# Performance work log

Hardware: AMD Instinct MI355X
Metric: run time of the kernel (lower is better)

The kernel has to match this reference:

```python
import jax, jax.numpy as jnp
import numpy as np

B, LQ, LA, D, H = 8, 2048, 2048, 300, 150

def setup_inputs() -> dict:
    key = jax.random.key(0)
    ks = jax.random.split(key, 6)
    return {
        "Q": jax.random.normal(ks[0], (B, LQ, D), dtype=jnp.float32),
        "A": jax.random.normal(ks[1], (B, LA, D), dtype=jnp.float32),
        "Wi": jax.random.normal(ks[2], (D, H), dtype=jnp.float32) * (1.0 / np.sqrt(D)),
        "Wu": jax.random.normal(ks[3], (D, H), dtype=jnp.float32) * (1.0 / np.sqrt(D)),
        "Wg": jax.random.normal(ks[4], (H, H), dtype=jnp.float32) * (1.0 / np.sqrt(H)),
        "Wt": jax.random.normal(ks[5], (2 * H, H), dtype=jnp.float32) * (1.0 / np.sqrt(2 * H)),
        "bi": jnp.zeros((H,), dtype=jnp.float32),
        "bu": jnp.zeros((H,), dtype=jnp.float32),
        "bg": jnp.zeros((H,), dtype=jnp.float32),
        "bt": jnp.zeros((H,), dtype=jnp.float32),
    }

def reference(Q, A, Wi, Wu, Wg, Wt, bi, bu, bg, bt):
    # sigmoid/tanh gated projections (shared weights for Q and A)
    def gate(X):
        return jax.nn.sigmoid(X @ Wi + bi) * jnp.tanh(X @ Wu + bu)
    Qh = gate(Q)  # [B, LQ, H]
    Ah = gate(A)  # [B, LA, H]
    # attention scores G[b,q,a] = <(Qh Wg + bg)[b,q], Ah[b,a]>
    G = jnp.einsum('bqh,bah->bqa', Qh @ Wg + bg, Ah)
    G = jax.nn.softmax(G, axis=1)  # softmax over Q positions
    # H[b,a] = sum_q G[b,q,a] * Qh[b,q]
    Hm = jnp.einsum('bqa,bqh->bah', G, Qh)  # [B, LA, H]
    # 'nn' comparison: relu(concat([Ah, Hm]) @ Wt + bt)
    T = jax.nn.relu(jnp.concatenate([Ah, Hm], axis=-1) @ Wt + bt)
    return T
```

## Files before the change

kernel.cpp:

```cpp
#include <hip/hip_runtime.h>
#include <math.h>

#define BB 8
#define LQ 2048
#define DD 300
#define HHH 150
#define NROWS (BB * LQ)

#define KP 168
#define QTS 72
#define XSS 328
#define WCE 27136
#define JT 144
#define SLAB_B 45056
#define SLAB_E 22528
#define QHT_OFF_E 11008

typedef __bf16 bf16x8 __attribute__((ext_vector_type(8)));
typedef __bf16 bf16x4 __attribute__((ext_vector_type(4)));
typedef float f32x16 __attribute__((ext_vector_type(16)));

__device__ __forceinline__ void gl_lds16(const void* g, void* l) {
    __builtin_amdgcn_global_load_lds(
        (const __attribute__((address_space(1))) void*)g,
        (__attribute__((address_space(3))) void*)l,
        16, 0, 0);
}
__device__ __forceinline__ void stage_flat(const void* g, void* l, int bytes,
                                           int w, int lane) {
    for (int ofs = w * 1024; ofs < bytes; ofs += 4096)
        gl_lds16((const char*)g + ofs + lane * 16, (char*)l + ofs);
}
__device__ __forceinline__ f32x16 z16() {
    f32x16 v;
#pragma unroll
    for (int i = 0; i < 16; i++) v[i] = 0.f;
    return v;
}

__global__ __launch_bounds__(256) void convert_weights(
    const float* __restrict__ Wi, const float* __restrict__ Wu,
    const float* __restrict__ Wg, const float* __restrict__ Wt,
    __bf16* __restrict__ WiC, __bf16* __restrict__ WuC,
    __bf16* __restrict__ WgT, __bf16* __restrict__ Wt12)
{
    const int z = blockIdx.y;
    const int i = blockIdx.x * 256 + threadIdx.x;
    if (z < 2) {
        if (i >= 2 * WCE) return;
        int c = i / WCE, rem = i - c * WCE;
        float v = 0.f;
        if (rem < 160 * KP) {
            int h = rem / KP, kc = rem - h * KP;
            int d = c * 160 + kc;
            if (kc < 160 && d < DD && h < HHH) v = (z ? Wu : Wi)[(size_t)d * HHH + h];
        }
        (z ? WuC : WiC)[i] = (__bf16)v;
    } else if (z == 2) {
        if (i >= WCE) return;
        float v = 0.f;
        if (i < 160 * KP) {
            int h = i / KP, kc = i - h * KP;
            if (kc < HHH && h < HHH) v = Wg[(size_t)kc * HHH + h];
        }
        WgT[i] = (__bf16)v;
    } else {
        if (i >= 2 * 160 * KP) return;
        int c = i / (160 * KP), rem = i - c * (160 * KP);
        int h = rem / KP, kc = rem - h * KP;
        float v = (kc < HHH && h < HHH) ? Wt[(size_t)(c * HHH + kc) * HHH + h] : 0.f;
        Wt12[i] = (__bf16)v;
    }
}

__global__ __launch_bounds__(256, 1) void gatep(
    const float* __restrict__ Q, const float* __restrict__ A,
    const __bf16* __restrict__ WiC, const __bf16* __restrict__ WuC,
    const __bf16* __restrict__ WgT,
    const float* __restrict__ bi, const float* __restrict__ bu,
    const float* __restrict__ bg,
    __bf16* __restrict__ AhB, __bf16* __restrict__ Slab)
{
    __shared__ __align__(16) __bf16 Xs[128 * XSS];
    __shared__ __align__(16) __bf16 WS[WCE];
    const int tid = threadIdx.x;
    const int w = tid >> 6, lane = tid & 63;
    const int m32 = lane & 31, half = lane >> 5;
    const int z = blockIdx.y;
    const int r0 = blockIdx.x * 128;
    const float* X = z ? A : Q;

    stage_flat(WiC, WS, 54272, w, lane);

    const float4* xs4 = (const float4*)(X + (size_t)r0 * DD);
    for (int i = tid; i < 9600; i += 256) {
        int row = i / 75, c4 = (i - row * 75) * 4;
        float4 v = xs4[i];
        *(bf16x4*)(Xs + row * XSS + c4) =
            (bf16x4){(__bf16)v.x, (__bf16)v.y, (__bf16)v.z, (__bf16)v.w};
    }
    for (int i = tid; i < 128 * 7; i += 256) {
        int row = i / 7, c4 = 300 + (i - row * 7) * 4;
        *(bf16x4*)(Xs + row * XSS + c4) =
            (bf16x4){(__bf16)0.f, (__bf16)0.f, (__bf16)0.f, (__bf16)0.f};
    }
    __syncthreads();

    f32x16 ai[5], au[5];
#pragma unroll
    for (int t = 0; t < 5; t++) { ai[t] = z16(); au[t] = z16(); }
    bf16x8 af[10];

    for (int c = 0; c < 2; c++) {
        if (c) { __syncthreads(); stage_flat(WiC + WCE, WS, 54272, w, lane); __syncthreads(); }
#pragma unroll
        for (int ks = 0; ks < 10; ks++)
            af[ks] = *(const bf16x8*)(Xs + (w * 32 + m32) * XSS + c * 160 + ks * 16 + half * 8);
        for (int ks = 0; ks < 10; ks++)
#pragma unroll
            for (int t = 0; t < 5; t++)
                ai[t] = __builtin_amdgcn_mfma_f32_32x32x16_bf16(
                    af[ks], *(const bf16x8*)(WS + (t * 32 + m32) * KP + ks * 16 + half * 8),
                    ai[t], 0, 0, 0);
        __syncthreads();
        stage_flat(WuC + (size_t)c * WCE, WS, 54272, w, lane);
        __syncthreads();
        for (int ks = 0; ks < 10; ks++)
#pragma unroll
            for (int t = 0; t < 5; t++)
                au[t] = __builtin_amdgcn_mfma_f32_32x32x16_bf16(
                    af[ks], *(const bf16x8*)(WS + (t * 32 + m32) * KP + ks * 16 + half * 8),
                    au[t], 0, 0, 0);
    }

#pragma unroll
    for (int t = 0; t < 5; t++) {
        int h = t * 32 + m32;
        int hc = h < HHH ? h : 0;
        float bih = bi[hc], buh = bu[hc];
#pragma unroll
        for (int r = 0; r < 16; r++) {
            float v = 0.f;
            if (h < HHH) {
                float xi = ai[t][r] + bih, xu = au[t][r] + buh;
                v = (1.f / (1.f + __expf(-xi))) * tanhf(xu);
            }
            ai[t][r] = v;
        }
    }

    if (z) {
#pragma unroll
        for (int t = 0; t < 5; t++) {
            int h = t * 32 + m32;
#pragma unroll
            for (int r = 0; r < 16; r++) {
                int rowp = (r & 3) + 8 * (r >> 2) + 4 * half;
                AhB[(size_t)(r0 + w * 32 + rowp) * KP + h] = (__bf16)ai[t][r];
            }
        }
        return;
    }

    __syncthreads();
#pragma unroll
    for (int t = 0; t < 5; t++) {
        int h = t * 32 + m32;
#pragma unroll
        for (int r = 0; r < 16; r++) {
            int rowp = (r & 3) + 8 * (r >> 2) + 4 * half;
            int j = w * 32 + rowp;
            __bf16 v = (__bf16)ai[t][r];
            Xs[j * KP + h] = v;
            WS[h * JT + j] = v;
        }
    }
    __syncthreads();
    const int b = r0 >> 11, qt0 = (r0 & 2047) >> 6;
    for (int i = tid; i < 2560; i += 256) {
        int tile = i / 1280, rr = i - tile * 1280;
        int hh = rr >> 3, seg = rr & 7;
        *(bf16x8*)(Slab + (size_t)(b * 32 + qt0 + tile) * SLAB_E + QHT_OFF_E + hh * QTS + seg * 8)
            = *(const bf16x8*)(WS + hh * JT + tile * 64 + seg * 8);
    }
    __syncthreads();
    stage_flat(WgT, WS, 54272, w, lane);
    __syncthreads();

    bf16x8 af2[10];
#pragma unroll
    for (int ks = 0; ks < 10; ks++)
        af2[ks] = *(const bf16x8*)(Xs + (w * 32 + m32) * KP + ks * 16 + half * 8);
    f32x16 qg[5];
#pragma unroll
    for (int t = 0; t < 5; t++) qg[t] = z16();
    for (int ks = 0; ks < 10; ks++)
#pragma unroll
        for (int t = 0; t < 5; t++)
            qg[t] = __builtin_amdgcn_mfma_f32_32x32x16_bf16(
                af2[ks], *(const bf16x8*)(WS + (t * 32 + m32) * KP + ks * 16 + half * 8),
                qg[t], 0, 0, 0);

#pragma unroll
    for (int t = 0; t < 5; t++) {
        int h = t * 32 + m32;
        int hc = h < HHH ? h : 0;
        float bgh = bg[hc];
#pragma unroll
        for (int r = 0; r < 16; r++) {
            int rowp = (r & 3) + 8 * (r >> 2) + 4 * half;
            int q = (r0 & 2047) + w * 32 + rowp;
            float v = (h < HHH) ? (qg[t][r] + bgh) : 0.f;
            Slab[(size_t)(b * 32 + (q >> 6)) * SLAB_E + (q & 63) * KP + h] = (__bf16)v;
        }
    }
}

__global__ __launch_bounds__(256, 1) void attn_mfma(
    const __bf16* __restrict__ Slab, const __bf16* __restrict__ AhB,
    __bf16* __restrict__ O, float* __restrict__ L)
{
    __shared__ __align__(16) __bf16 AhS[128 * KP];
    __shared__ __align__(16) __bf16 Buf[2][SLAB_E];
    __shared__ __align__(16) __bf16 PS[128 * QTS];
    const int tid = threadIdx.x;
    const int w = tid >> 6, lane = tid & 63;
    const int m32 = lane & 31, half = lane >> 5;
    const int b = blockIdx.y, qh = blockIdx.z;
    const int a0 = blockIdx.x * 128;

    stage_flat(AhB + (size_t)(b * LQ + a0) * KP, AhS, 43008, w, lane);
    const char* slabBase = (const char*)Slab + (size_t)(b * 32 + qh * 16) * SLAB_B;
    stage_flat(slabBase, Buf[0], SLAB_B, w, lane);
    __syncthreads();

    bf16x8 af[10];
#pragma unroll
    for (int ks = 0; ks < 10; ks++)
        af[ks] = *(const bf16x8*)(AhS + (w * 32 + m32) * KP + ks * 16 + half * 8);

    float lsum[16];
#pragma unroll
    for (int r = 0; r < 16; r++) lsum[r] = 0.f;
    f32x16 acc[5];
#pragma unroll
    for (int t = 0; t < 5; t++) acc[t] = z16();

    for (int qt = 0; qt < 16; qt++) {
        const int cur = qt & 1;
        if (qt < 15)
            stage_flat(slabBase + (size_t)(qt + 1) * SLAB_B, Buf[cur ^ 1], SLAB_B, w, lane);
        const __bf16* Bq = Buf[cur];
        const __bf16* Bv = Buf[cur] + QHT_OFF_E;

        f32x16 s0 = z16(), s1 = z16();
        for (int ks = 0; ks < 10; ks++) {
            s0 = __builtin_amdgcn_mfma_f32_32x32x16_bf16(
                af[ks], *(const bf16x8*)(Bq + m32 * KP + ks * 16 + half * 8), s0, 0, 0, 0);
            s1 = __builtin_amdgcn_mfma_f32_32x32x16_bf16(
                af[ks], *(const bf16x8*)(Bq + (32 + m32) * KP + ks * 16 + half * 8), s1, 0, 0, 0);
        }
#pragma unroll
        for (int r = 0; r < 16; r++) {
            int rowp = (r & 3) + 8 * (r >> 2) + 4 * half;
            float p0 = __expf(s0[r]);
            float p1 = __expf(s1[r]);
            lsum[r] += p0 + p1;
            PS[(w * 32 + rowp) * QTS + m32] = (__bf16)p0;
            PS[(w * 32 + rowp) * QTS + 32 + m32] = (__bf16)p1;
        }
#pragma unroll
        for (int kk = 0; kk < 4; kk++) {
            bf16x8 pf = *(const bf16x8*)(PS + (w * 32 + m32) * QTS + kk * 16 + half * 8);
#pragma unroll
            for (int t = 0; t < 5; t++)
                acc[t] = __builtin_amdgcn_mfma_f32_32x32x16_bf16(
                    pf, *(const bf16x8*)(Bv + (t * 32 + m32) * QTS + kk * 16 + half * 8),
                    acc[t], 0, 0, 0);
        }
        __syncthreads();
    }

#pragma unroll
    for (int r = 0; r < 16; r++) {
        float s = lsum[r];
#pragma unroll
        for (int m = 1; m < 32; m <<= 1) s += __shfl_xor(s, m, 64);
        lsum[r] = s;
    }
    __bf16* Ob = O + (size_t)(qh * NROWS + b * LQ + a0) * 160;
#pragma unroll
    for (int t = 0; t < 5; t++) {
        int h = t * 32 + m32;
#pragma unroll
        for (int r = 0; r < 16; r++) {
            int rowp = (r & 3) + 8 * (r >> 2) + 4 * half;
            Ob[(size_t)(w * 32 + rowp) * 160 + h] = (__bf16)acc[t][r];
        }
    }
    if (m32 == 0) {
        float* Lb = L + qh * NROWS + b * LQ + a0 + w * 32;
#pragma unroll
        for (int r = 0; r < 16; r++) {
            int rowp = (r & 3) + 8 * (r >> 2) + 4 * half;
            Lb[rowp] = lsum[r];
        }
    }
}

__global__ __launch_bounds__(256, 1) void final_mfma(
    const __bf16* __restrict__ AhB, const __bf16* __restrict__ O,
    const float* __restrict__ L, const __bf16* __restrict__ Wt12,
    const float* __restrict__ bt, float* __restrict__ Out)
{
    __shared__ __align__(16) __bf16 AS[64 * KP];
    __shared__ __align__(16) __bf16 HS[64 * KP];
    __shared__ __align__(16) __bf16 WtS[2 * 160 * KP];
    const int tid = threadIdx.x;
    const int w = tid >> 6, lane = tid & 63;
    const int m32 = lane & 31, half = lane >> 5;
    const int r0 = blockIdx.x * 64;

    stage_flat(AhB + (size_t)r0 * KP, AS, 21504, w, lane);
    stage_flat(Wt12, WtS, 107520, w, lane);

    {
        int rhat = tid >> 2, qq = tid & 3;
        int grow = r0 + rhat;
        float inv = 1.f / (L[grow] + L[NROWS + grow]);
        const bf16x8* o1 = (const bf16x8*)(O + (size_t)grow * 160 + qq * 40);
        const bf16x8* o2 = (const bf16x8*)(O + (size_t)(NROWS + grow) * 160 + qq * 40);
#pragma unroll
        for (int k = 0; k < 5; k++) {
            bf16x8 x = o1[k], y = o2[k], hv;
#pragma unroll
            for (int j = 0; j < 8; j++)
                hv[j] = (__bf16)(((float)x[j] + (float)y[j]) * inv);
            *(bf16x8*)(HS + rhat * KP + qq * 40 + k * 8) = hv;
        }
    }
    __syncthreads();

    const int m = w & 1, th = w >> 1;
    const int tbase = th ? 3 : 0, tn = th ? 2 : 3;
    f32x16 acc[3];
#pragma unroll
    for (int i = 0; i < 3; i++) acc[i] = z16();

    for (int ch = 0; ch < 2; ch++) {
        const __bf16* src = ch ? HS : AS;
        for (int ks = 0; ks < 10; ks++) {
            bf16x8 af = *(const bf16x8*)(src + (m * 32 + m32) * KP + ks * 16 + half * 8);
#pragma unroll
            for (int ti = 0; ti < 3; ti++) {
                if (ti < tn) {
                    int t = tbase + ti;
                    acc[ti] = __builtin_amdgcn_mfma_f32_32x32x16_bf16(
                        af, *(const bf16x8*)(WtS + (ch * 160 + t * 32 + m32) * KP + ks * 16 + half * 8),
                        acc[ti], 0, 0, 0);
                }
            }
        }
    }

#pragma unroll
    for (int ti = 0; ti < 3; ti++) {
        if (ti < tn) {
            int t = tbase + ti;
            int h = t * 32 + m32;
            if (h < HHH) {
                float bth = bt[h];
#pragma unroll
                for (int r = 0; r < 16; r++) {
                    int rowp = (r & 3) + 8 * (r >> 2) + 4 * half;
                    float v = acc[ti][r] + bth;
                    Out[(size_t)(r0 + m * 32 + rowp) * HHH + h] = v > 0.f ? v : 0.f;
                }
            }
        }
    }
}

extern "C" void kernel_launch(void* const* d_in, const int* in_sizes, int n_in,
                              void* d_out, int out_size, void* d_ws, size_t ws_size,
                              hipStream_t stream)
{
    const float* Q  = (const float*)d_in[0];
    const float* A  = (const float*)d_in[1];
    const float* Wi = (const float*)d_in[2];
    const float* Wu = (const float*)d_in[3];
    const float* Wg = (const float*)d_in[4];
    const float* Wt = (const float*)d_in[5];
    const float* bi = (const float*)d_in[6];
    const float* bu = (const float*)d_in[7];
    const float* bg = (const float*)d_in[8];
    const float* bt = (const float*)d_in[9];
    float* out = (float*)d_out;

    char* ws = (char*)d_ws;
    __bf16* Slab = (__bf16*)(ws);
    __bf16* AhB  = (__bf16*)(ws + 11534336);
    __bf16* Op   = (__bf16*)(ws + 17039360);
    float*  Lp   = (float*) (ws + 27525120);
    __bf16* WiC  = (__bf16*)(ws + 27656192);
    __bf16* WuC  = (__bf16*)(ws + 27764736);
    __bf16* WgT  = (__bf16*)(ws + 27873280);
    __bf16* Wt12 = (__bf16*)(ws + 27927552);

    convert_weights<<<dim3(212, 4), 256, 0, stream>>>(Wi, Wu, Wg, Wt,
                                                      WiC, WuC, WgT, Wt12);
    gatep<<<dim3(NROWS / 128, 2), 256, 0, stream>>>(Q, A, WiC, WuC, WgT,
                                                    bi, bu, bg, AhB, Slab);
    attn_mfma<<<dim3(16, BB, 2), 256, 0, stream>>>(Slab, AhB, Op, Lp);
    final_mfma<<<NROWS / 64, 256, 0, stream>>>(AhB, Op, Lp, Wt12, bt, out);
}
```

Baseline: 188.5 us.

## Double-buffer gate weights in LDS and load X fragments directly into registers

The gatep kernel now streams X rows straight from global memory into bf16 MFMA fragments instead of staging them through a padded LDS tile. Wi, Wu and Wg chunks are double-buffered in two LDS slabs, so the next weight chunk loads while the current one is used in MFMAs, and several barriers are dropped. tanh is replaced by an exp-based formula, and the transposed Qh slab is written from a single LDS copy with scattered stores. The risks are higher register pressure from holding 20 fragments, uncoalesced direct global loads, and strided 2-byte scatter stores for the transpose.

```diff
diff --git a/kernel.cpp b/kernel.cpp
--- a/kernel.cpp
+++ b/kernel.cpp
@@ -9,9 +9,7 @@
 
 #define KP 168
 #define QTS 72
-#define XSS 328
 #define WCE 27136
-#define JT 144
 #define SLAB_B 45056
 #define SLAB_E 22528
 #define QHT_OFF_E 11008
@@ -36,6 +34,10 @@
 #pragma unroll
     for (int i = 0; i < 16; i++) v[i] = 0.f;
     return v;
+}
+__device__ __forceinline__ bf16x8 cvt8(float4 u, float4 v) {
+    return (bf16x8){(__bf16)u.x, (__bf16)u.y, (__bf16)u.z, (__bf16)u.w,
+                    (__bf16)v.x, (__bf16)v.y, (__bf16)v.z, (__bf16)v.w};
 }
 
 __global__ __launch_bounds__(256) void convert_weights(
@@ -81,8 +83,8 @@
     const float* __restrict__ bg,
     __bf16* __restrict__ AhB, __bf16* __restrict__ Slab)
 {
-    __shared__ __align__(16) __bf16 Xs[128 * XSS];
-    __shared__ __align__(16) __bf16 WS[WCE];
+    __shared__ __align__(16) __bf16 WB[2][WCE];
+    __shared__ __align__(16) __bf16 QhA[128 * KP];
     const int tid = threadIdx.x;
     const int w = tid >> 6, lane = tid & 63;
     const int m32 = lane & 31, half = lane >> 5;
@@ -90,48 +92,68 @@
     const int r0 = blockIdx.x * 128;
     const float* X = z ? A : Q;
 
-    stage_flat(WiC, WS, 54272, w, lane);
-
-    const float4* xs4 = (const float4*)(X + (size_t)r0 * DD);
-    for (int i = tid; i < 9600; i += 256) {
-        int row = i / 75, c4 = (i - row * 75) * 4;
-        float4 v = xs4[i];
-        *(bf16x4*)(Xs + row * XSS + c4) =
-            (bf16x4){(__bf16)v.x, (__bf16)v.y, (__bf16)v.z, (__bf16)v.w};
-    }
-    for (int i = tid; i < 128 * 7; i += 256) {
-        int row = i / 7, c4 = 300 + (i - row * 7) * 4;
-        *(bf16x4*)(Xs + row * XSS + c4) =
-            (bf16x4){(__bf16)0.f, (__bf16)0.f, (__bf16)0.f, (__bf16)0.f};
-    }
-    __syncthreads();
+    stage_flat(WiC, WB[0], 54272, w, lane);
+
+    const float* xrow = X + (size_t)(r0 + w * 32 + m32) * DD + half * 8;
+    bf16x8 af0[10], af1[10];
+#pragma unroll
+    for (int ks = 0; ks < 10; ks++) {
+        float4 u = *(const float4*)(xrow + ks * 16);
+        float4 v = *(const float4*)(xrow + ks * 16 + 4);
+        af0[ks] = cvt8(u, v);
+    }
 
     f32x16 ai[5], au[5];
 #pragma unroll
     for (int t = 0; t < 5; t++) { ai[t] = z16(); au[t] = z16(); }
-    bf16x8 af[10];
-
-    for (int c = 0; c < 2; c++) {
-        if (c) { __syncthreads(); stage_flat(WiC + WCE, WS, 54272, w, lane); __syncthreads(); }
-#pragma unroll
-        for (int ks = 0; ks < 10; ks++)
-            af[ks] = *(const bf16x8*)(Xs + (w * 32 + m32) * XSS + c * 160 + ks * 16 + half * 8);
-        for (int ks = 0; ks < 10; ks++)
-#pragma unroll
-            for (int t = 0; t < 5; t++)
-                ai[t] = __builtin_amdgcn_mfma_f32_32x32x16_bf16(
-                    af[ks], *(const bf16x8*)(WS + (t * 32 + m32) * KP + ks * 16 + half * 8),
-                    ai[t], 0, 0, 0);
-        __syncthreads();
-        stage_flat(WuC + (size_t)c * WCE, WS, 54272, w, lane);
-        __syncthreads();
-        for (int ks = 0; ks < 10; ks++)
-#pragma unroll
-            for (int t = 0; t < 5; t++)
-                au[t] = __builtin_amdgcn_mfma_f32_32x32x16_bf16(
-                    af[ks], *(const bf16x8*)(WS + (t * 32 + m32) * KP + ks * 16 + half * 8),
-                    au[t], 0, 0, 0);
-    }
+
+    __syncthreads();
+    stage_flat(WuC, WB[1], 54272, w, lane);
+
+#pragma unroll
+    for (int ks = 0; ks < 8; ks++) {
+        float4 u = *(const float4*)(xrow + 160 + ks * 16);
+        float4 v = *(const float4*)(xrow + 160 + ks * 16 + 4);
+        af1[ks] = cvt8(u, v);
+    }
+    {
+        float4 u = *(const float4*)(xrow + 288);
+        float4 v = (half == 0) ? *(const float4*)(xrow + 292) : (float4){0.f, 0.f, 0.f, 0.f};
+        af1[8] = cvt8(u, v);
+        af1[9] = (bf16x8){(__bf16)0.f, (__bf16)0.f, (__bf16)0.f, (__bf16)0.f,
+                          (__bf16)0.f, (__bf16)0.f, (__bf16)0.f, (__bf16)0.f};
+    }
+
+    for (int ks = 0; ks < 10; ks++)
+#pragma unroll
+        for (int t = 0; t < 5; t++)
+            ai[t] = __builtin_amdgcn_mfma_f32_32x32x16_bf16(
+                af0[ks], *(const bf16x8*)(WB[0] + (t * 32 + m32) * KP + ks * 16 + half * 8),
+                ai[t], 0, 0, 0);
+    __syncthreads();
+    stage_flat(WiC + WCE, WB[0], 54272, w, lane);
+    for (int ks = 0; ks < 10; ks++)
+#pragma unroll
+        for (int t = 0; t < 5; t++)
+            au[t] = __builtin_amdgcn_mfma_f32_32x32x16_bf16(
+                af0[ks], *(const bf16x8*)(WB[1] + (t * 32 + m32) * KP + ks * 16 + half * 8),
+                au[t], 0, 0, 0);
+    __syncthreads();
+    stage_flat(WuC + WCE, WB[1], 54272, w, lane);
+    for (int ks = 0; ks < 10; ks++)
+#pragma unroll
+        for (int t = 0; t < 5; t++)
+            ai[t] = __builtin_amdgcn_mfma_f32_32x32x16_bf16(
+                af1[ks], *(const bf16x8*)(WB[0] + (t * 32 + m32) * KP + ks * 16 + half * 8),
+                ai[t], 0, 0, 0);
+    __syncthreads();
+    if (z == 0) stage_flat(WgT, WB[0], 54272, w, lane);
+    for (int ks = 0; ks < 10; ks++)
+#pragma unroll
+        for (int t = 0; t < 5; t++)
+            au[t] = __builtin_amdgcn_mfma_f32_32x32x16_bf16(
+                af1[ks], *(const bf16x8*)(WB[1] + (t * 32 + m32) * KP + ks * 16 + half * 8),
+                au[t], 0, 0, 0);
 
 #pragma unroll
     for (int t = 0; t < 5; t++) {
@@ -143,7 +165,9 @@
             float v = 0.f;
             if (h < HHH) {
                 float xi = ai[t][r] + bih, xu = au[t][r] + buh;
-                v = (1.f / (1.f + __expf(-xi))) * tanhf(xu);
+                float s = 1.f / (1.f + __expf(-xi));
+                float tt = 1.f - 2.f / (1.f + __expf(2.f * xu));
+                v = s * tt;
             }
             ai[t][r] = v;
         }
@@ -162,35 +186,21 @@
         return;
     }
 
-    __syncthreads();
 #pragma unroll
     for (int t = 0; t < 5; t++) {
         int h = t * 32 + m32;
 #pragma unroll
         for (int r = 0; r < 16; r++) {
             int rowp = (r & 3) + 8 * (r >> 2) + 4 * half;
-            int j = w * 32 + rowp;
-            __bf16 v = (__bf16)ai[t][r];
-            Xs[j * KP + h] = v;
-            WS[h * JT + j] = v;
-        }
-    }
-    __syncthreads();
-    const int b = r0 >> 11, qt0 = (r0 & 2047) >> 6;
-    for (int i = tid; i < 2560; i += 256) {
-        int tile = i / 1280, rr = i - tile * 1280;
-        int hh = rr >> 3, seg = rr & 7;
-        *(bf16x8*)(Slab + (size_t)(b * 32 + qt0 + tile) * SLAB_E + QHT_OFF_E + hh * QTS + seg * 8)
-            = *(const bf16x8*)(WS + hh * JT + tile * 64 + seg * 8);
-    }
-    __syncthreads();
-    stage_flat(WgT, WS, 54272, w, lane);
-    __syncthreads();
-
-    bf16x8 af2[10];
-#pragma unroll
-    for (int ks = 0; ks < 10; ks++)
-        af2[ks] = *(const bf16x8*)(Xs + (w * 32 + m32) * KP + ks * 16 + half * 8);
+            QhA[(w * 32 + rowp) * KP + h] = (__bf16)ai[t][r];
+        }
+    }
+    bf16x8 afq[10];
+#pragma unroll
+    for (int ks = 0; ks < 10; ks++)
+        afq[ks] = *(const bf16x8*)(QhA + (w * 32 + m32) * KP + ks * 16 + half * 8);
+    __syncthreads();
+
     f32x16 qg[5];
 #pragma unroll
     for (int t = 0; t < 5; t++) qg[t] = z16();
@@ -198,9 +208,10 @@
 #pragma unroll
         for (int t = 0; t < 5; t++)
             qg[t] = __builtin_amdgcn_mfma_f32_32x32x16_bf16(
-                af2[ks], *(const bf16x8*)(WS + (t * 32 + m32) * KP + ks * 16 + half * 8),
+                afq[ks], *(const bf16x8*)(WB[0] + (t * 32 + m32) * KP + ks * 16 + half * 8),
                 qg[t], 0, 0, 0);
 
+    const int b = r0 >> 11, qt0 = (r0 & 2047) >> 6;
 #pragma unroll
     for (int t = 0; t < 5; t++) {
         int h = t * 32 + m32;
@@ -212,6 +223,17 @@
             int q = (r0 & 2047) + w * 32 + rowp;
             float v = (h < HHH) ? (qg[t][r] + bgh) : 0.f;
             Slab[(size_t)(b * 32 + (q >> 6)) * SLAB_E + (q & 63) * KP + h] = (__bf16)v;
+        }
+    }
+
+    {
+        const int jl = tid & 63, tile = (tid >> 6) & 1, hgrp = tid >> 7;
+        for (int hseg = hgrp; hseg < 20; hseg += 2) {
+            bf16x8 vv = *(const bf16x8*)(QhA + (tile * 64 + jl) * KP + hseg * 8);
+            __bf16* dst = Slab + (size_t)(b * 32 + qt0 + tile) * SLAB_E + QHT_OFF_E + jl;
+#pragma unroll
+            for (int e = 0; e < 8; e++)
+                dst[(hseg * 8 + e) * QTS] = vv[e];
         }
     }
 }
```

Result: faster. 169.1 us (-10.3%).
